# Performance work log

Hardware: AMD Instinct MI355X
Metric: run time of the kernel (lower is better)

## Reference

```python
import jax, jax.numpy as jnp
import numpy as np


def setup_inputs() -> dict:
    key = jax.random.key(0)
    k1, k2, k3 = jax.random.split(key, 3)
    B, N, D, S = 256, 200000, 128, 256
    return {
        "query": jax.random.normal(k1, (B, D), dtype=jnp.float32),
        "keys": jax.random.normal(k2, (N, D), dtype=jnp.float32),
        "slots": jax.random.normal(k3, (N, S), dtype=jnp.float32),
        "k": 8,
    }


def reference(query, keys, slots, k):
    # FAISS IndexFlatIP exact search: inner-product scores over all stored keys.
    scores = jnp.einsum("bd,nd->bn", query, keys)          # [B, N]
    top_scores, top_idx = jax.lax.top_k(scores, k)          # [B, k]
    # Fused id->slot gather (replaces per-(query,neighbor) equality scans).
    retrieved_slots = slots[top_idx]                        # [B, k, slot_dim]
    return retrieved_slots, top_scores
```

## Files before the change

### kernel.cpp

```cpp
#include <hip/hip_runtime.h>

#define NQ    256
#define DD    128
#define NK    200000
#define SD    256
#define KTOP  8
#define CAP   1024

#define NCH   500
#define CHK   400
#define KST   80
#define NST   (CHK/KST)
#define KT    (KST/16)
#define BUFB  (KST*256)
static_assert(NCH * CHK == NK, "chunking must cover keys");

#define WS_A    0
#define WS_TAUF 65536
#define WS_TAU  66560
#define WS_CNT  67584
#define WS_CAND 69632

#define NEG_INF (-3.402823466e+38f)

typedef __attribute__((ext_vector_type(8))) short short8;
typedef __attribute__((ext_vector_type(4))) float f32x4;

__device__ __forceinline__ unsigned f2bf(float f) {
    unsigned u = __float_as_uint(f);
    u += 0x7fffu + ((u >> 16) & 1u);
    return u >> 16;
}

__device__ __forceinline__ float dot128(const float4* __restrict__ qr,
                                        const float4* __restrict__ kr) {
    float s0 = 0.f, s1 = 0.f;
#pragma unroll
    for (int d = 0; d < 16; ++d) {
        float4 a = qr[d], b = kr[d];
        s0 = fmaf(a.x, b.x, s0); s0 = fmaf(a.y, b.y, s0);
        s0 = fmaf(a.z, b.z, s0); s0 = fmaf(a.w, b.w, s0);
    }
#pragma unroll
    for (int d = 16; d < 32; ++d) {
        float4 a = qr[d], b = kr[d];
        s1 = fmaf(a.x, b.x, s1); s1 = fmaf(a.y, b.y, s1);
        s1 = fmaf(a.z, b.z, s1); s1 = fmaf(a.w, b.w, s1);
    }
    return s0 + s1;
}

template <int T>
__device__ __forceinline__ void topk_insert(float (&vs)[T], int (&vi)[T],
                                            float &vmin, float s, int idx) {
    if (s <= vmin) return;
    bool done = false;
#pragma unroll
    for (int j = 0; j < T; ++j)
        if (!done && vs[j] == vmin) { vs[j] = s; vi[j] = idx; done = true; }
    float m = vs[0];
#pragma unroll
    for (int j = 1; j < T; ++j) m = fminf(m, vs[j]);
    vmin = m;
}

__device__ void finalize_write(int q, int t, float (&vs)[KTOP], int (&vi)[KTOP],
                               float vmin, float* ds, int* di,
                               const float* __restrict__ slots,
                               float* __restrict__ out) {
#pragma unroll
    for (int j = 0; j < KTOP; ++j) { ds[t * KTOP + j] = vs[j]; di[t * KTOP + j] = vi[j]; }
    __syncthreads();
    for (int step = 128; step >= 1; step >>= 1) {
        if (t < step) {
            for (int j = 0; j < KTOP; ++j)
                topk_insert<KTOP>(vs, vi, vmin, ds[(t + step) * KTOP + j],
                                  di[(t + step) * KTOP + j]);
#pragma unroll
            for (int j = 0; j < KTOP; ++j) { ds[t * KTOP + j] = vs[j]; di[t * KTOP + j] = vi[j]; }
        }
        __syncthreads();
    }
    if (t == 0) {
#pragma unroll
        for (int i = 0; i < KTOP; ++i)
#pragma unroll
            for (int j = 0; j < KTOP - 1 - i; ++j) {
                bool swp = (vs[j + 1] > vs[j]) ||
                           (vs[j + 1] == vs[j] && vi[j + 1] < vi[j]);
                if (swp) {
                    float tf = vs[j]; vs[j] = vs[j + 1]; vs[j + 1] = tf;
                    int   ti = vi[j]; vi[j] = vi[j + 1]; vi[j + 1] = ti;
                }
            }
#pragma unroll
        for (int j = 0; j < KTOP; ++j) { ds[j] = vs[j]; di[j] = vi[j]; }
    }
    __syncthreads();
    const float4* slots4 = (const float4*)slots;
    float4* out4 = (float4*)out;
    for (int f = t; f < KTOP * (SD / 4); f += 256) {
        int j = f >> 6, s4 = f & 63;
        out4[(size_t)q * (KTOP * SD / 4) + f] = slots4[(size_t)di[j] * (SD / 4) + s4];
    }
    if (t < KTOP)
        out[(size_t)NQ * KTOP * SD + q * KTOP + t] = ds[t];
}

__global__ __launch_bounds__(256) void prep(const float* __restrict__ query,
                                            char* __restrict__ ws) {
    __shared__ float qs[16 * DD];
    __shared__ float nrm[16][17];
    const int b = blockIdx.x, t = threadIdx.x;

    const float4* src = (const float4*)(query + (size_t)b * 16 * DD);
    float4* dst = (float4*)qs;
    for (int i = t; i < 512; i += 256) dst[i] = src[i];
    __syncthreads();

    {
        int r = t >> 4, p = t & 15;
        float s = 0.f;
#pragma unroll
        for (int j = 0; j < 8; ++j) { float v = qs[r * DD + p * 8 + j]; s = fmaf(v, v, s); }
        nrm[r][p] = s;
    }
    __syncthreads();
    if (t < 16) {
        float s = 0.f;
#pragma unroll
        for (int p = 0; p < 16; ++p) s += nrm[t][p];
        float tau = 3.2f * sqrtf(s);
        ((float*)(ws + WS_TAU))[b * 16 + t]  = tau;
        ((float*)(ws + WS_TAUF))[b * 16 + t] = tau - 1.0f;
    }
    if (b == 0) ((int*)(ws + WS_CNT))[t] = 0;

    {
        int c = t >> 6, l = t & 63, col = l & 15, quad = l >> 4;
        const float* row = qs + col * DD + c * 32 + quad * 8;
        int4 pk;
        pk.x = f2bf(row[0]) | (f2bf(row[1]) << 16);
        pk.y = f2bf(row[2]) | (f2bf(row[3]) << 16);
        pk.z = f2bf(row[4]) | (f2bf(row[5]) << 16);
        pk.w = f2bf(row[6]) | (f2bf(row[7]) << 16);
        ((int4*)(ws + WS_A))[(b * 4 + c) * 64 + l] = pk;
    }
}

__global__ __launch_bounds__(256, 2)
void phaseA(const float* __restrict__ keys, char* __restrict__ ws) {
    __shared__ __align__(16) char sm[2 * BUFB];

    const int tid = threadIdx.x;
    const int w = tid >> 6, lane = tid & 63;
    const int col = lane & 15, quad = lane >> 4;
    const int key0 = blockIdx.x * CHK;

    const short8* wsA = (const short8*)(ws + WS_A);
    short8 A[4][4];
#pragma unroll
    for (int at = 0; at < 4; ++at)
#pragma unroll
        for (int c = 0; c < 4; ++c)
            A[at][c] = wsA[((w * 4 + at) * 4 + c) * 64 + lane];

    const float* tauf = (const float*)(ws + WS_TAUF);
    float tf[4][4];
#pragma unroll
    for (int at = 0; at < 4; ++at)
#pragma unroll
        for (int r = 0; r < 4; ++r)
            tf[at][r] = tauf[w * 64 + at * 16 + quad * 4 + r];

    int* cnt  = (int*)(ws + WS_CNT);
    int* cand = (int*)(ws + WS_CAND);

    float4 rg[5][2];

#define LOAD_STAGE(S)                                                          \
    {                                                                          \
        _Pragma("unroll")                                                      \
        for (int i = 0; i < 5; ++i) {                                          \
            int u = tid + 256 * i, tc = u >> 6, l = u & 63;                    \
            const float* p = keys +                                            \
                (size_t)(key0 + (S) * KST + (tc >> 2) * 16 + (l & 15)) * DD +  \
                (tc & 3) * 32 + (l >> 4) * 8;                                  \
            rg[i][0] = ((const float4*)p)[0];                                  \
            rg[i][1] = ((const float4*)p)[1];                                  \
        }                                                                      \
    }
#define WRITE_STAGE(BUF)                                                       \
    {                                                                          \
        _Pragma("unroll")                                                      \
        for (int i = 0; i < 5; ++i) {                                          \
            int u = tid + 256 * i;                                             \
            int4 pk;                                                           \
            pk.x = f2bf(rg[i][0].x) | (f2bf(rg[i][0].y) << 16);                \
            pk.y = f2bf(rg[i][0].z) | (f2bf(rg[i][0].w) << 16);                \
            pk.z = f2bf(rg[i][1].x) | (f2bf(rg[i][1].y) << 16);                \
            pk.w = f2bf(rg[i][1].z) | (f2bf(rg[i][1].w) << 16);                \
            *(int4*)(sm + (size_t)(BUF) * BUFB + (size_t)u * 16) = pk;         \
        }                                                                      \
    }

    LOAD_STAGE(0);
    WRITE_STAGE(0);
    __syncthreads();

    for (int s = 0; s < NST; ++s) {
        if (s + 1 < NST) LOAD_STAGE(s + 1);
        const short8* B = (const short8*)(sm + (s & 1) * BUFB);
#pragma unroll
        for (int kt = 0; kt < KT; ++kt) {
            short8 b0 = B[(kt * 4 + 0) * 64 + lane];
            short8 b1 = B[(kt * 4 + 1) * 64 + lane];
            short8 b2 = B[(kt * 4 + 2) * 64 + lane];
            short8 b3 = B[(kt * 4 + 3) * 64 + lane];
            const int kidx = key0 + s * KST + kt * 16 + col;
#pragma unroll
            for (int at = 0; at < 4; ++at) {
                f32x4 acc = {0.f, 0.f, 0.f, 0.f};
                acc = __builtin_amdgcn_mfma_f32_16x16x32_bf16(A[at][0], b0, acc, 0, 0, 0);
                acc = __builtin_amdgcn_mfma_f32_16x16x32_bf16(A[at][1], b1, acc, 0, 0, 0);
                acc = __builtin_amdgcn_mfma_f32_16x16x32_bf16(A[at][2], b2, acc, 0, 0, 0);
                acc = __builtin_amdgcn_mfma_f32_16x16x32_bf16(A[at][3], b3, acc, 0, 0, 0);
#pragma unroll
                for (int r = 0; r < 4; ++r) {
                    if (acc[r] > tf[at][r]) {
                        int q = w * 64 + at * 16 + quad * 4 + r;
                        int p = atomicAdd(&cnt[q], 1);
                        if (p < CAP) cand[q * CAP + p] = kidx;
                    }
                }
            }
        }
        if (s + 1 < NST) {
            WRITE_STAGE((s + 1) & 1);
            __syncthreads();
        }
    }
#undef LOAD_STAGE
#undef WRITE_STAGE
}

__global__ __launch_bounds__(256)
void phaseB(const float* __restrict__ query, const float* __restrict__ keys,
            const float* __restrict__ slots, float* __restrict__ out,
            char* __restrict__ ws) {
    const int q = blockIdx.x, t = threadIdx.x;

    __shared__ float cs[CAP];
    __shared__ int   ci[CAP];
    __shared__ int   nAbove;
    __shared__ float ds[256 * KTOP];
    __shared__ int   di[256 * KTOP];

    if (t == 0) nAbove = 0;
    __syncthreads();

    const int m0 = ((const int*)(ws + WS_CNT))[q];
    const int m  = min(m0, CAP);
    const float tq = ((const float*)(ws + WS_TAU))[q];
    const int* cand = (const int*)(ws + WS_CAND) + (size_t)q * CAP;
    const float4* qr = (const float4*)(query + (size_t)q * DD);

    int myAbove = 0;
    for (int c = t; c < m; c += 256) {
        int id = cand[c];
        float s = dot128(qr, (const float4*)(keys + (size_t)id * DD));
        cs[c] = s; ci[c] = id;
        if (s >= tq) ++myAbove;
    }
    if (myAbove) atomicAdd(&nAbove, myAbove);
    __syncthreads();

    float vs[KTOP]; int vi[KTOP]; float vmin = NEG_INF;
#pragma unroll
    for (int j = 0; j < KTOP; ++j) { vs[j] = NEG_INF; vi[j] = -1; }

    if (m0 > CAP || nAbove < KTOP) {
        for (int id = t; id < NK; id += 256) {
            float s = dot128(qr, (const float4*)(keys + (size_t)id * DD));
            topk_insert<KTOP>(vs, vi, vmin, s, id);
        }
    } else {
        for (int c = t; c < m; c += 256)
            topk_insert<KTOP>(vs, vi, vmin, cs[c], ci[c]);
    }

    finalize_write(q, t, vs, vi, vmin, ds, di, slots, out);
}

extern "C" void kernel_launch(void* const* d_in, const int* in_sizes, int n_in,
                              void* d_out, int out_size, void* d_ws, size_t ws_size,
                              hipStream_t stream) {
    const float* query = (const float*)d_in[0];
    const float* keys  = (const float*)d_in[1];
    const float* slots = (const float*)d_in[2];
    (void)in_sizes; (void)n_in; (void)out_size; (void)ws_size;
    char* ws = (char*)d_ws;

    hipLaunchKernelGGL(prep,   dim3(16),  dim3(256), 0, stream, query, ws);
    hipLaunchKernelGGL(phaseA, dim3(NCH), dim3(256), 0, stream, keys, ws);
    hipLaunchKernelGGL(phaseB, dim3(NQ),  dim3(256), 0, stream, query, keys, slots,
                       (float*)d_out, ws);
}
```

Measured before the change: 365.2 us.

## Fuse prep, phaseA, phaseB into one cooperative kernel with grid syncs

Merges the three kernels into a single cooperative launch that uses grid-wide syncs between phases. This removes the launch gaps and the drain and refill between kernels, with a fallback to three separate launches if residency is insufficient. It also adds a per-tile max-versus-min-threshold pre-check so the per-row atomic branches are skipped in the common case. The fused kernel keeps 500 blocks resident, but the phaseB work runs on only 256 of them, and grid syncs have their own cost.

```diff
diff --git a/kernel.cpp b/kernel.cpp
--- a/kernel.cpp
+++ b/kernel.cpp
@@ -1,4 +1,6 @@
 #include <hip/hip_runtime.h>
+#include <hip/hip_cooperative_groups.h>
+namespace cg = cooperative_groups;
 
 #define NQ    256
 #define DD    128
@@ -107,11 +109,10 @@
         out[(size_t)NQ * KTOP * SD + q * KTOP + t] = ds[t];
 }
 
-__global__ __launch_bounds__(256) void prep(const float* __restrict__ query,
-                                            char* __restrict__ ws) {
-    __shared__ float qs[16 * DD];
-    __shared__ float nrm[16][17];
-    const int b = blockIdx.x, t = threadIdx.x;
+__device__ void prep_body(int b, int t, const float* __restrict__ query,
+                          char* __restrict__ ws, char* sm) {
+    float* qs = (float*)sm;
+    float (*nrm)[17] = (float (*)[17])(sm + 8192);
 
     const float4* src = (const float4*)(query + (size_t)b * 16 * DD);
     float4* dst = (float4*)qs;
@@ -148,14 +149,11 @@
     }
 }
 
-__global__ __launch_bounds__(256, 2)
-void phaseA(const float* __restrict__ keys, char* __restrict__ ws) {
-    __shared__ __align__(16) char sm[2 * BUFB];
-
-    const int tid = threadIdx.x;
+__device__ void phaseA_body(int blk, int tid, const float* __restrict__ keys,
+                            char* __restrict__ ws, char* sm) {
     const int w = tid >> 6, lane = tid & 63;
     const int col = lane & 15, quad = lane >> 4;
-    const int key0 = blockIdx.x * CHK;
+    const int key0 = blk * CHK;
 
     const short8* wsA = (const short8*)(ws + WS_A);
     short8 A[4][4];
@@ -166,12 +164,14 @@
             A[at][c] = wsA[((w * 4 + at) * 4 + c) * 64 + lane];
 
     const float* tauf = (const float*)(ws + WS_TAUF);
-    float tf[4][4];
-#pragma unroll
-    for (int at = 0; at < 4; ++at)
+    float tf[4][4], tfmin[4];
+#pragma unroll
+    for (int at = 0; at < 4; ++at) {
 #pragma unroll
         for (int r = 0; r < 4; ++r)
             tf[at][r] = tauf[w * 64 + at * 16 + quad * 4 + r];
+        tfmin[at] = fminf(fminf(tf[at][0], tf[at][1]), fminf(tf[at][2], tf[at][3]));
+    }
 
     int* cnt  = (int*)(ws + WS_CNT);
     int* cand = (int*)(ws + WS_CAND);
@@ -225,12 +225,15 @@
                 acc = __builtin_amdgcn_mfma_f32_16x16x32_bf16(A[at][1], b1, acc, 0, 0, 0);
                 acc = __builtin_amdgcn_mfma_f32_16x16x32_bf16(A[at][2], b2, acc, 0, 0, 0);
                 acc = __builtin_amdgcn_mfma_f32_16x16x32_bf16(A[at][3], b3, acc, 0, 0, 0);
-#pragma unroll
-                for (int r = 0; r < 4; ++r) {
-                    if (acc[r] > tf[at][r]) {
-                        int q = w * 64 + at * 16 + quad * 4 + r;
-                        int p = atomicAdd(&cnt[q], 1);
-                        if (p < CAP) cand[q * CAP + p] = kidx;
+                float mx = fmaxf(fmaxf(acc[0], acc[1]), fmaxf(acc[2], acc[3]));
+                if (mx > tfmin[at]) {
+#pragma unroll
+                    for (int r = 0; r < 4; ++r) {
+                        if (acc[r] > tf[at][r]) {
+                            int q = w * 64 + at * 16 + quad * 4 + r;
+                            int p = atomicAdd(&cnt[q], 1);
+                            if (p < CAP) cand[q * CAP + p] = kidx;
+                        }
                     }
                 }
             }
@@ -244,19 +247,18 @@
 #undef WRITE_STAGE
 }
 
-__global__ __launch_bounds__(256)
-void phaseB(const float* __restrict__ query, const float* __restrict__ keys,
-            const float* __restrict__ slots, float* __restrict__ out,
-            char* __restrict__ ws) {
-    const int q = blockIdx.x, t = threadIdx.x;
-
-    __shared__ float cs[CAP];
-    __shared__ int   ci[CAP];
-    __shared__ int   nAbove;
-    __shared__ float ds[256 * KTOP];
-    __shared__ int   di[256 * KTOP];
-
-    if (t == 0) nAbove = 0;
+__device__ void phaseB_body(int q, int t, const float* __restrict__ query,
+                            const float* __restrict__ keys,
+                            const float* __restrict__ slots,
+                            float* __restrict__ out, char* __restrict__ ws,
+                            char* sm) {
+    float* cs = (float*)sm;
+    int*   ci = (int*)(sm + 4096);
+    float* ds = (float*)(sm + 8192);
+    int*   di = (int*)(sm + 16384);
+    int* nAbove = (int*)(sm + 24576);
+
+    if (t == 0) *nAbove = 0;
     __syncthreads();
 
     const int m0 = ((const int*)(ws + WS_CNT))[q];
@@ -272,14 +274,14 @@
         cs[c] = s; ci[c] = id;
         if (s >= tq) ++myAbove;
     }
-    if (myAbove) atomicAdd(&nAbove, myAbove);
+    if (myAbove) atomicAdd(nAbove, myAbove);
     __syncthreads();
 
     float vs[KTOP]; int vi[KTOP]; float vmin = NEG_INF;
 #pragma unroll
     for (int j = 0; j < KTOP; ++j) { vs[j] = NEG_INF; vi[j] = -1; }
 
-    if (m0 > CAP || nAbove < KTOP) {
+    if (m0 > CAP || *nAbove < KTOP) {
         for (int id = t; id < NK; id += 256) {
             float s = dot128(qr, (const float4*)(keys + (size_t)id * DD));
             topk_insert<KTOP>(vs, vi, vmin, s, id);
@@ -292,17 +294,70 @@
     finalize_write(q, t, vs, vi, vmin, ds, di, slots, out);
 }
 
+__global__ __launch_bounds__(256, 2)
+void fused(const float* __restrict__ query, const float* __restrict__ keys,
+           const float* __restrict__ slots, float* __restrict__ out,
+           char* __restrict__ ws) {
+    __shared__ __align__(16) char sm[2 * BUFB];
+    cg::grid_group g = cg::this_grid();
+
+    if (blockIdx.x < 16) prep_body(blockIdx.x, threadIdx.x, query, ws, sm);
+    __threadfence();
+    g.sync();
+    __threadfence();
+
+    phaseA_body(blockIdx.x, threadIdx.x, keys, ws, sm);
+    __threadfence();
+    g.sync();
+    __threadfence();
+
+    if (blockIdx.x < NQ)
+        phaseB_body(blockIdx.x, threadIdx.x, query, keys, slots, out, ws, sm);
+}
+
+__global__ __launch_bounds__(256) void prep_k(const float* __restrict__ query,
+                                              char* __restrict__ ws) {
+    __shared__ __align__(16) char sm[9280];
+    prep_body(blockIdx.x, threadIdx.x, query, ws, sm);
+}
+__global__ __launch_bounds__(256, 2) void phaseA_k(const float* __restrict__ keys,
+                                                   char* __restrict__ ws) {
+    __shared__ __align__(16) char sm[2 * BUFB];
+    phaseA_body(blockIdx.x, threadIdx.x, keys, ws, sm);
+}
+__global__ __launch_bounds__(256) void phaseB_k(const float* __restrict__ query,
+                                                const float* __restrict__ keys,
+                                                const float* __restrict__ slots,
+                                                float* __restrict__ out,
+                                                char* __restrict__ ws) {
+    __shared__ __align__(16) char sm[24704];
+    phaseB_body(blockIdx.x, threadIdx.x, query, keys, slots, out, ws, sm);
+}
+
 extern "C" void kernel_launch(void* const* d_in, const int* in_sizes, int n_in,
                               void* d_out, int out_size, void* d_ws, size_t ws_size,
                               hipStream_t stream) {
     const float* query = (const float*)d_in[0];
     const float* keys  = (const float*)d_in[1];
     const float* slots = (const float*)d_in[2];
+    float* outp = (float*)d_out;
+    char*  ws   = (char*)d_ws;
     (void)in_sizes; (void)n_in; (void)out_size; (void)ws_size;
-    char* ws = (char*)d_ws;
-
-    hipLaunchKernelGGL(prep,   dim3(16),  dim3(256), 0, stream, query, ws);
-    hipLaunchKernelGGL(phaseA, dim3(NCH), dim3(256), 0, stream, keys, ws);
-    hipLaunchKernelGGL(phaseB, dim3(NQ),  dim3(256), 0, stream, query, keys, slots,
-                       (float*)d_out, ws);
-}
+
+    int maxBlk = 0;
+    hipError_t qe = hipOccupancyMaxActiveBlocksPerMultiprocessor(
+        &maxBlk, (const void*)fused, 256, 0);
+    bool coop = (qe == hipSuccess) && ((long)maxBlk * 256 >= NCH);
+
+    if (coop) {
+        void* args[5] = {(void*)&query, (void*)&keys, (void*)&slots,
+                         (void*)&outp, (void*)&ws};
+        hipError_t e = hipLaunchCooperativeKernel((const void*)fused, dim3(NCH),
+                                                  dim3(256), args, 0, stream);
+        if (e == hipSuccess) return;
+    }
+    hipLaunchKernelGGL(prep_k,   dim3(16),  dim3(256), 0, stream, query, ws);
+    hipLaunchKernelGGL(phaseA_k, dim3(NCH), dim3(256), 0, stream, keys, ws);
+    hipLaunchKernelGGL(phaseB_k, dim3(NQ),  dim3(256), 0, stream, query, keys, slots,
+                       outp, ws);
+}
```

Measured after the change: 378.4 us. 3.6% more time.
